# Kernel tuning notes

Measured on AMD Instinct MI355X. Metric: run time of the kernel, lower is better.

Reference implementation:

```python
import jax, jax.numpy as jnp
import numpy as np
from jax import lax

EPS = 1e-05


def rmsnorm_axis1(x, w, eps=EPS):
    # RMS over channel axis (axis=1), scale by per-channel weight
    ms = jnp.mean(x * x, axis=1, keepdims=True)
    return x * lax.rsqrt(ms + eps) * w[None, :, None]


def dwconv1d(x, w, b, dilation):
    # x: [B, C, L]; w: [C, 1, K] depthwise (feature_group_count=C)
    pad = (w.shape[-1] - 1) // 2 * dilation
    y = lax.conv_general_dilated(
        x, w, window_strides=(1,), padding=[(pad, pad)],
        rhs_dilation=(dilation,), dimension_numbers=('NCH', 'OIH', 'NCH'),
        feature_group_count=x.shape[1])
    return y + b[None, :, None]


def setup_inputs() -> dict:
    key = jax.random.key(0)
    ks = jax.random.split(key, 12)
    B, C, L, K = 16, 512, 2048, 3
    s = 1.0 / np.sqrt(C)
    return {
        'number_log': jax.random.normal(ks[0], (B,), jnp.float32),
        'x': jax.random.normal(ks[1], (B, C, L), jnp.float32),
        'pre_w': jnp.ones((C,), jnp.float32),
        'conv_w': jax.random.normal(ks[2], (C, 1, K), jnp.float32) * 0.3,
        'conv_b': jnp.zeros((C,), jnp.float32),
        'conv1_w': jax.random.normal(ks[3], (C, 1, K), jnp.float32) * 0.3,
        'conv1_b': jnp.zeros((C,), jnp.float32),
        'conv2_w': jax.random.normal(ks[4], (C, 1, K), jnp.float32) * 0.3,
        'conv2_b': jnp.zeros((C,), jnp.float32),
        'gate_w': jax.random.normal(ks[5], (C, C), jnp.float32) * s,
        'gate_b': jnp.zeros((C,), jnp.float32),
        'post_w': jnp.ones((C,), jnp.float32),
        'logits_w': jax.random.normal(ks[6], (1, C, 1), jnp.float32) * s,
    }


def reference(number_log, x, pre_w, conv_w, conv_b, conv1_w, conv1_b,
              conv2_w, conv2_b, gate_w, gate_b, post_w, logits_w):
    # pre_norm over channel axis
    x_norm = rmsnorm_axis1(x, pre_w)
    # three dilated depthwise conv branches, summed
    x_d = (dwconv1d(x_norm, conv_w, conv_b, 1)
           + dwconv1d(x_norm, conv1_w, conv1_b, 2)
           + dwconv1d(x_norm, conv2_w, conv2_b, 4))
    # gate: Linear over channel dim of transposed input, SiLU
    gate = jax.nn.silu(jnp.einsum('bcl,dc->bdl', x_norm, gate_w)
                       + gate_b[None, :, None])
    x_d = rmsnorm_axis1(x_d * gate, post_w)
    # logits: 1x1 conv C->1, no bias
    out = jnp.einsum('bcl,oc->bol', x + x_d, logits_w[:, :, 0])
    return out
```

## Files before the change

kernel.cpp:

```cpp
#include <hip/hip_runtime.h>
#include <hip/hip_bf16.h>

#define BB 16
#define CC 512
#define LL 2048

typedef float f32x4 __attribute__((ext_vector_type(4)));
typedef short s16x8 __attribute__((ext_vector_type(8)));

static __device__ __forceinline__ float bf2f(unsigned short u) {
    union { unsigned int i; float f; } v; v.i = ((unsigned int)u) << 16; return v.f;
}
static __device__ __forceinline__ unsigned short f2bf(float f) {
    union { float fv; unsigned int i; } v; v.fv = f;
    unsigned int x = v.i;
    return (unsigned short)((x + 0x7FFFu + ((x >> 16) & 1u)) >> 16);
}

__global__ void k0_cast(const float* __restrict__ gw, unsigned short* __restrict__ gwb) {
    int i = blockIdx.x * 256 + threadIdx.x;
    if (i < CC * CC) gwb[i] = f2bf(gw[i]);
}

#define K1_ST 520
__global__ __launch_bounds__(256) void k1_rms_t(
    const float* __restrict__ x, const float* __restrict__ pre_w,
    unsigned short* __restrict__ xnt, float* __restrict__ invr) {
    __shared__ unsigned short tile[32 * K1_ST];
    __shared__ float red[32 * 33];
    __shared__ float pwS[CC];
    __shared__ float ivS[32];
    const int tid = threadIdx.x;
    const int b  = blockIdx.x >> 6;
    const int lt = blockIdx.x & 63;
    const int l0 = lt * 32;
    const float* xb = x + (size_t)(b * CC) * LL + l0;

    for (int i = tid; i < CC; i += 256) pwS[i] = pre_w[i];

    const int lq = tid & 7;
    const int cr = tid >> 3;
    f32x4 ssq = {0.f, 0.f, 0.f, 0.f};
    #pragma unroll
    for (int p = 0; p < 16; ++p) {
        int c = p * 32 + cr;
        f32x4 v = *(const f32x4*)(xb + (size_t)c * LL + lq * 4);
        #pragma unroll
        for (int r = 0; r < 4; ++r) {
            ssq[r] += v[r] * v[r];
            tile[(lq * 4 + r) * K1_ST + c] = f2bf(v[r]);
        }
    }
    #pragma unroll
    for (int r = 0; r < 4; ++r) red[(lq * 4 + r) * 33 + cr] = ssq[r];
    __syncthreads();
    if (tid < 32) {
        float s = 0.f;
        #pragma unroll
        for (int g = 0; g < 32; ++g) s += red[tid * 33 + g];
        float iv = rsqrtf(s * (1.0f / CC) + 1e-5f);
        ivS[tid] = iv;
        invr[b * LL + l0 + tid] = iv;
    }
    __syncthreads();
    unsigned short* xo = xnt + ((size_t)b * LL + l0) * CC;
    #pragma unroll
    for (int p = 0; p < 8; ++p) {
        int g = p * 256 + tid;
        int l = g >> 6, c8 = (g & 63) * 8;
        s16x8 t = *(const s16x8*)&tile[l * K1_ST + c8];
        f32x4 w0 = *(const f32x4*)&pwS[c8];
        f32x4 w1 = *(const f32x4*)&pwS[c8 + 4];
        float iv = ivS[l];
        s16x8 o;
        #pragma unroll
        for (int r = 0; r < 4; ++r) {
            o[r]     = (short)f2bf(bf2f((unsigned short)t[r])     * iv * w0[r]);
            o[r + 4] = (short)f2bf(bf2f((unsigned short)t[r + 4]) * iv * w1[r]);
        }
        *(s16x8*)(xo + (size_t)l * CC + c8) = o;
    }
}

__global__ __launch_bounds__(512, 2) void k2_gemm(
    const unsigned short* __restrict__ gwb,
    const unsigned short* __restrict__ xnt,
    const float* __restrict__ gate_b,
    unsigned short* __restrict__ gate) {
    __shared__ unsigned short As[3][256 * 32];
    __shared__ unsigned short Bs[3][256 * 32];
    const int tid = threadIdx.x;
    const int w = tid >> 6, lane = tid & 63;
    const int lo = lane & 15, hi = lane >> 4;
    const int wm = w >> 2, wn = w & 3;
    const int nt = blockIdx.x, mt = blockIdx.y, b = blockIdx.z;
    const int m0 = mt * 256, n0 = nt * 256;
    const unsigned short* Ab = gwb;
    const unsigned short* Bb = xnt + (size_t)b * LL * CC;

    #define STG(kt_, buf_)                                                            \
        {                                                                             \
            _Pragma("unroll")                                                         \
            for (int s_ = 0; s_ < 2; ++s_) {                                          \
                int g_ = tid + s_ * 512;                                              \
                int row_ = g_ >> 2, gin_ = g_ & 3;                                    \
                int ks_ = (kt_) * 32 + ((gin_ ^ ((row_ >> 1) & 3)) * 8);              \
                __builtin_amdgcn_global_load_lds(                                     \
                    (const __attribute__((address_space(1))) void*)(Ab + (size_t)(m0 + row_) * CC + ks_), \
                    (__attribute__((address_space(3))) void*)(&As[buf_][g_ * 8]),     \
                    16, 0, 0);                                                        \
                __builtin_amdgcn_global_load_lds(                                     \
                    (const __attribute__((address_space(1))) void*)(Bb + (size_t)(n0 + row_) * CC + ks_), \
                    (__attribute__((address_space(3))) void*)(&Bs[buf_][g_ * 8]),     \
                    16, 0, 0);                                                        \
            }                                                                         \
        }

    f32x4 acc[8][4] = {};
    const int fsw = (lo >> 1) & 3;

    STG(0, 0);
    STG(1, 1);
    #pragma unroll
    for (int kt = 0; kt < 16; ++kt) {
        const int buf = kt % 3;
        if (kt < 14) {
            STG(kt + 2, (kt + 2) % 3);
            asm volatile("s_waitcnt vmcnt(8)" ::: "memory");
        } else if (kt == 14) {
            asm volatile("s_waitcnt vmcnt(4)" ::: "memory");
        } else {
            asm volatile("s_waitcnt vmcnt(0)" ::: "memory");
        }
        __builtin_amdgcn_s_barrier();
        s16x8 af[8], bfr[4];
        #pragma unroll
        for (int mi = 0; mi < 8; ++mi)
            af[mi] = *(const s16x8*)&As[buf][(wm * 128 + mi * 16 + lo) * 32 + ((hi ^ fsw) * 8)];
        #pragma unroll
        for (int ni = 0; ni < 4; ++ni)
            bfr[ni] = *(const s16x8*)&Bs[buf][(wn * 64 + ni * 16 + lo) * 32 + ((hi ^ fsw) * 8)];
        __builtin_amdgcn_s_setprio(1);
        #pragma unroll
        for (int mi = 0; mi < 8; ++mi)
            #pragma unroll
            for (int ni = 0; ni < 4; ++ni)
                acc[mi][ni] = __builtin_amdgcn_mfma_f32_16x16x32_bf16(
                    af[mi], bfr[ni], acc[mi][ni], 0, 0, 0);
        __builtin_amdgcn_s_setprio(0);
        asm volatile("" ::: "memory");
        __builtin_amdgcn_s_barrier();
    }
    #undef STG

    #pragma unroll
    for (int mi = 0; mi < 8; ++mi) {
        #pragma unroll
        for (int ni = 0; ni < 4; ++ni) {
            int n = n0 + wn * 64 + ni * 16 + lo;
            int d0 = m0 + wm * 128 + mi * 16 + hi * 4;
            #pragma unroll
            for (int r = 0; r < 4; ++r) {
                int d = d0 + r;
                float z = acc[mi][ni][r] + gate_b[d];
                float s = z / (1.0f + __expf(-z));
                gate[((size_t)(b * CC + d)) * LL + n] = f2bf(s);
            }
        }
    }
}

__global__ __launch_bounds__(256) void k3a(
    const float* __restrict__ x, const float* __restrict__ invr,
    const unsigned short* __restrict__ gate,
    const float* __restrict__ cw0, const float* __restrict__ cb0,
    const float* __restrict__ cw1, const float* __restrict__ cb1,
    const float* __restrict__ cw2, const float* __restrict__ cb2,
    const float* __restrict__ pre_w, const float* __restrict__ post_w,
    const float* __restrict__ lw, float* __restrict__ part) {
    __shared__ float tapS[64][8];
    __shared__ float biasS[64], preS[64], lwS[64], pwlwS[64];
    __shared__ float ivs[136];
    __shared__ float red[8][128][3];
    const int tid = threadIdx.x;
    const int lt = blockIdx.x;
    const int cc = blockIdx.y;
    const int b  = blockIdx.z;
    const int l0 = lt * 128;
    const int c0 = cc * 64;

    if (tid < 64) {
        int c = c0 + tid;
        float w10 = cw0[c*3], w11 = cw0[c*3+1], w12 = cw0[c*3+2];
        float w20 = cw1[c*3], w21 = cw1[c*3+1], w22 = cw1[c*3+2];
        float w40 = cw2[c*3], w41 = cw2[c*3+1], w42 = cw2[c*3+2];
        tapS[tid][0] = w40; tapS[tid][1] = w20; tapS[tid][2] = w10;
        tapS[tid][3] = w11 + w21 + w41;
        tapS[tid][4] = w12; tapS[tid][5] = w22; tapS[tid][6] = w42;
        biasS[tid] = cb0[c] + cb1[c] + cb2[c];
        preS[tid]  = pre_w[c];
        float lwc = lw[c];
        lwS[tid] = lwc;
        pwlwS[tid] = post_w[c] * lwc;
    }
    if (tid < 136) {
        int lg = l0 - 4 + tid;
        ivs[tid] = (lg >= 0 && lg < LL) ? invr[b * LL + lg] : 0.f;
    }
    __syncthreads();

    const int li = tid & 31, ci = tid >> 5;
    const int lq = l0 + li * 4;
    float iv[12];
    #pragma unroll
    for (int j = 0; j < 12; ++j) iv[j] = ivs[li * 4 + j];

    const int ia = (lq - 4 < 0) ? 0 : lq - 4;
    const int ic = (lq + 4 > LL - 4) ? LL - 4 : lq + 4;

    float ass[4] = {}, adp[4] = {}, adx[4] = {};
    const float* xbase = x + ((size_t)(b * CC + c0)) * LL;
    const unsigned short* gbase = gate + ((size_t)(b * CC + c0)) * LL;

    #pragma unroll
    for (int j = 0; j < 8; ++j) {
        const int cl = ci * 8 + j;
        const float* xr = xbase + (size_t)cl * LL;
        f32x4 xa = *(const f32x4*)(xr + ia);
        f32x4 xm = *(const f32x4*)(xr + lq);
        f32x4 xc = *(const f32x4*)(xr + ic);
        uint2 gu = *(const uint2*)(gbase + (size_t)cl * LL + lq);
        float g[4];
        g[0] = bf2f((unsigned short)(gu.x & 0xffff));
        g[1] = bf2f((unsigned short)(gu.x >> 16));
        g[2] = bf2f((unsigned short)(gu.y & 0xffff));
        g[3] = bf2f((unsigned short)(gu.y >> 16));
        float z[12];
        #pragma unroll
        for (int r = 0; r < 4; ++r) {
            z[r]     = xa[r] * iv[r];
            z[r + 4] = xm[r] * iv[r + 4];
            z[r + 8] = xc[r] * iv[r + 8];
        }
        const float t0 = tapS[cl][0], t1 = tapS[cl][1], t2 = tapS[cl][2],
                    t3 = tapS[cl][3], t4 = tapS[cl][4], t5 = tapS[cl][5],
                    t6 = tapS[cl][6];
        const float pre = preS[cl], bias = biasS[cl], pwlw = pwlwS[cl], lwc = lwS[cl];
        #pragma unroll
        for (int k = 0; k < 4; ++k) {
            float s = t0 * z[k] + t1 * z[k + 2] + t2 * z[k + 3] + t3 * z[k + 4]
                    + t4 * z[k + 5] + t5 * z[k + 6] + t6 * z[k + 8];
            float p = (pre * s + bias) * g[k];
            ass[k] += p * p;
            adp[k] += p * pwlw;
            adx[k] += xm[k] * lwc;
        }
    }
    #pragma unroll
    for (int k = 0; k < 4; ++k) {
        red[ci][li * 4 + k][0] = ass[k];
        red[ci][li * 4 + k][1] = adp[k];
        red[ci][li * 4 + k][2] = adx[k];
    }
    __syncthreads();
    if (tid < 128) {
        float s0 = 0.f, s1 = 0.f, s2 = 0.f;
        #pragma unroll
        for (int g2 = 0; g2 < 8; ++g2) {
            s0 += red[g2][tid][0];
            s1 += red[g2][tid][1];
            s2 += red[g2][tid][2];
        }
        float* pp = part + (((size_t)(b * 8 + cc)) * LL + l0 + tid) * 3;
        pp[0] = s0; pp[1] = s1; pp[2] = s2;
    }
}

__global__ __launch_bounds__(256) void k3b(
    const float* __restrict__ part, float* __restrict__ out) {
    int gl = blockIdx.x * 256 + threadIdx.x;
    int b = gl >> 11, l = gl & 2047;
    float s0 = 0.f, s1 = 0.f, s2 = 0.f;
    #pragma unroll
    for (int cc2 = 0; cc2 < 8; ++cc2) {
        const float* pp = part + (((size_t)(b * 8 + cc2)) * LL + l) * 3;
        s0 += pp[0]; s1 += pp[1]; s2 += pp[2];
    }
    out[gl] = s2 + rsqrtf(s0 * (1.0f / CC) + 1e-5f) * s1;
}

extern "C" void kernel_launch(void* const* d_in, const int* in_sizes, int n_in,
                              void* d_out, int out_size, void* d_ws, size_t ws_size,
                              hipStream_t stream) {
    const float* x      = (const float*)d_in[1];
    const float* pre_w  = (const float*)d_in[2];
    const float* cw0    = (const float*)d_in[3];
    const float* cb0    = (const float*)d_in[4];
    const float* cw1    = (const float*)d_in[5];
    const float* cb1    = (const float*)d_in[6];
    const float* cw2    = (const float*)d_in[7];
    const float* cb2    = (const float*)d_in[8];
    const float* gw     = (const float*)d_in[9];
    const float* gb     = (const float*)d_in[10];
    const float* post_w = (const float*)d_in[11];
    const float* lw     = (const float*)d_in[12];
    float* out = (float*)d_out;

    char* ws = (char*)d_ws;
    unsigned short* gwb  = (unsigned short*)(ws);
    unsigned short* xnt  = (unsigned short*)(ws + 524288);
    float*          invr = (float*)(ws + 524288 + 33554432);
    unsigned short* gate = (unsigned short*)(ws + 524288 + 33554432 + 131072);
    float*          part = (float*)(ws + 524288);

    hipLaunchKernelGGL(k0_cast,  dim3((CC * CC + 255) / 256), dim3(256), 0, stream, gw, gwb);
    hipLaunchKernelGGL(k1_rms_t, dim3(BB * (LL / 32)),        dim3(256), 0, stream, x, pre_w, xnt, invr);
    hipLaunchKernelGGL(k2_gemm,  dim3(LL / 256, CC / 256, BB), dim3(512), 0, stream, gwb, xnt, gb, gate);
    hipLaunchKernelGGL(k3a,      dim3(LL / 128, CC / 64, BB), dim3(256), 0, stream,
                       x, invr, gate, cw0, cb0, cw1, cb1, cw2, cb2, pre_w, post_w, lw, part);
    hipLaunchKernelGGL(k3b,      dim3(BB * LL / 256),         dim3(256), 0, stream, part, out);
}
```

Baseline: 78.64 us.

## Restructure gate GEMM into 8-phase pipeline with K=64 tiles and interleaved staging

Replaces the triple-buffered K=32 main loop of the gate GEMM with double-buffered K=64 tiles split into half-tiles. Each K-step runs as four phases, and each phase loads a slice of A fragments, issues one global-to-LDS stage, and performs a burst of MFMAs. This spreads memory issue across compute phases, widens the XOR LDS swizzle to 8 groups, and halves the number of barrier-delimited K iterations per tile. The cost is more barriers per K-step and tighter hand-tuned vmcnt accounting, which risks hazards if the counts are wrong.

```diff
diff --git a/kernel.cpp b/kernel.cpp
--- a/kernel.cpp
+++ b/kernel.cpp
@@ -87,8 +87,8 @@
     const unsigned short* __restrict__ xnt,
     const float* __restrict__ gate_b,
     unsigned short* __restrict__ gate) {
-    __shared__ unsigned short As[3][256 * 32];
-    __shared__ unsigned short Bs[3][256 * 32];
+    __shared__ unsigned short Ash[2][2][128 * 64];
+    __shared__ unsigned short Bsh[2][2][128 * 64];
     const int tid = threadIdx.x;
     const int w = tid >> 6, lane = tid & 63;
     const int lo = lane & 15, hi = lane >> 4;
@@ -98,60 +98,94 @@
     const unsigned short* Ab = gwb;
     const unsigned short* Bb = xnt + (size_t)b * LL * CC;
 
-    #define STG(kt_, buf_)                                                            \
+    const int srow = tid >> 3;
+    const int skg  = tid & 7;
+
+    #define STGA(d_, h_, kt_)                                                         \
+        { _Pragma("unroll")                                                           \
+          for (int s_ = 0; s_ < 2; ++s_) {                                            \
+              int row_ = srow + s_ * 64;                                              \
+              __builtin_amdgcn_global_load_lds(                                       \
+                  (const __attribute__((address_space(1))) void*)(Ab + (size_t)(m0 + (h_) * 128 + row_) * CC + (kt_) * 64 + ((skg ^ (row_ & 7)) * 8)), \
+                  (__attribute__((address_space(3))) void*)(&Ash[d_][h_][(row_ * 8 + skg) * 8]), \
+                  16, 0, 0);                                                          \
+          } }
+    #define STGB(d_, h_, kt_)                                                         \
+        { _Pragma("unroll")                                                           \
+          for (int s_ = 0; s_ < 2; ++s_) {                                            \
+              int row_ = srow + s_ * 64;                                              \
+              __builtin_amdgcn_global_load_lds(                                       \
+                  (const __attribute__((address_space(1))) void*)(Bb + (size_t)(n0 + (h_) * 128 + row_) * CC + (kt_) * 64 + ((skg ^ (row_ & 7)) * 8)), \
+                  (__attribute__((address_space(3))) void*)(&Bsh[d_][h_][(row_ * 8 + skg) * 8]), \
+                  16, 0, 0);                                                          \
+          } }
+
+    f32x4 acc[8][4] = {};
+
+    STGA(0, 0, 0); STGA(0, 1, 0);
+    STGB(0, 0, 0); STGB(0, 1, 0);
+    STGB(1, 0, 1); STGB(1, 1, 1);
+    asm volatile("s_waitcnt vmcnt(0)" ::: "memory");
+    __builtin_amdgcn_s_barrier();
+
+    #define PHASE(d_, q_, STAGE_STMT, VM_STMT)                                        \
         {                                                                             \
+            s16x8 af_[2][2];                                                          \
             _Pragma("unroll")                                                         \
-            for (int s_ = 0; s_ < 2; ++s_) {                                          \
-                int g_ = tid + s_ * 512;                                              \
-                int row_ = g_ >> 2, gin_ = g_ & 3;                                    \
-                int ks_ = (kt_) * 32 + ((gin_ ^ ((row_ >> 1) & 3)) * 8);              \
-                __builtin_amdgcn_global_load_lds(                                     \
-                    (const __attribute__((address_space(1))) void*)(Ab + (size_t)(m0 + row_) * CC + ks_), \
-                    (__attribute__((address_space(3))) void*)(&As[buf_][g_ * 8]),     \
-                    16, 0, 0);                                                        \
-                __builtin_amdgcn_global_load_lds(                                     \
-                    (const __attribute__((address_space(1))) void*)(Bb + (size_t)(n0 + row_) * CC + ks_), \
-                    (__attribute__((address_space(3))) void*)(&Bs[buf_][g_ * 8]),     \
-                    16, 0, 0);                                                        \
+            for (int j_ = 0; j_ < 2; ++j_) {                                          \
+                int lr_ = ((q_) * 2 + j_) * 16 + lo;                                  \
+                _Pragma("unroll")                                                     \
+                for (int kk_ = 0; kk_ < 2; ++kk_)                                     \
+                    af_[j_][kk_] = *(const s16x8*)&Ash[d_][wm][lr_ * 64 + (((kk_ * 4 + hi) ^ (lr_ & 7)) * 8)]; \
             }                                                                         \
-        }
-
-    f32x4 acc[8][4] = {};
-    const int fsw = (lo >> 1) & 3;
-
-    STG(0, 0);
-    STG(1, 1);
-    #pragma unroll
-    for (int kt = 0; kt < 16; ++kt) {
-        const int buf = kt % 3;
-        if (kt < 14) {
-            STG(kt + 2, (kt + 2) % 3);
-            asm volatile("s_waitcnt vmcnt(8)" ::: "memory");
-        } else if (kt == 14) {
-            asm volatile("s_waitcnt vmcnt(4)" ::: "memory");
-        } else {
-            asm volatile("s_waitcnt vmcnt(0)" ::: "memory");
-        }
-        __builtin_amdgcn_s_barrier();
-        s16x8 af[8], bfr[4];
-        #pragma unroll
-        for (int mi = 0; mi < 8; ++mi)
-            af[mi] = *(const s16x8*)&As[buf][(wm * 128 + mi * 16 + lo) * 32 + ((hi ^ fsw) * 8)];
-        #pragma unroll
-        for (int ni = 0; ni < 4; ++ni)
-            bfr[ni] = *(const s16x8*)&Bs[buf][(wn * 64 + ni * 16 + lo) * 32 + ((hi ^ fsw) * 8)];
-        __builtin_amdgcn_s_setprio(1);
-        #pragma unroll
-        for (int mi = 0; mi < 8; ++mi)
-            #pragma unroll
-            for (int ni = 0; ni < 4; ++ni)
-                acc[mi][ni] = __builtin_amdgcn_mfma_f32_16x16x32_bf16(
-                    af[mi], bfr[ni], acc[mi][ni], 0, 0, 0);
-        __builtin_amdgcn_s_setprio(0);
-        asm volatile("" ::: "memory");
-        __builtin_amdgcn_s_barrier();
-    }
-    #undef STG
+            if ((q_) == 0) {                                                          \
+                _Pragma("unroll")                                                     \
+                for (int ni_ = 0; ni_ < 4; ++ni_) {                                   \
+                    int gr_ = wn * 64 + ni_ * 16 + lo;                                \
+                    int lr_ = gr_ & 127;                                              \
+                    _Pragma("unroll")                                                 \
+                    for (int kk_ = 0; kk_ < 2; ++kk_)                                 \
+                        bfr[ni_][kk_] = *(const s16x8*)&Bsh[d_][gr_ >> 7][lr_ * 64 + (((kk_ * 4 + hi) ^ (lr_ & 7)) * 8)]; \
+                }                                                                     \
+            }                                                                         \
+            STAGE_STMT;                                                               \
+            __builtin_amdgcn_s_barrier();                                             \
+            asm volatile("s_waitcnt lgkmcnt(0)" ::: "memory");                        \
+            __builtin_amdgcn_sched_barrier(0);                                        \
+            __builtin_amdgcn_s_setprio(1);                                            \
+            _Pragma("unroll")                                                         \
+            for (int j_ = 0; j_ < 2; ++j_)                                            \
+                _Pragma("unroll")                                                     \
+                for (int ni_ = 0; ni_ < 4; ++ni_)                                     \
+                    _Pragma("unroll")                                                 \
+                    for (int kk_ = 0; kk_ < 2; ++kk_)                                 \
+                        acc[(q_) * 2 + j_][ni_] = __builtin_amdgcn_mfma_f32_16x16x32_bf16( \
+                            af_[j_][kk_], bfr[ni_][kk_], acc[(q_) * 2 + j_][ni_], 0, 0, 0); \
+            __builtin_amdgcn_s_setprio(0);                                            \
+            VM_STMT;                                                                  \
+            __builtin_amdgcn_s_barrier();                                             \
+        }
+
+    #define VM4  asm volatile("s_waitcnt vmcnt(4)" ::: "memory")
+    #define VM0  asm volatile("s_waitcnt vmcnt(0)" ::: "memory")
+
+    #pragma unroll
+    for (int I = 0; I < 4; ++I) {
+        s16x8 bfr[4][2];
+        PHASE(0, 0, STGA(1, 0, 2 * I + 1), );
+        PHASE(0, 1, STGA(1, 1, 2 * I + 1), );
+        PHASE(0, 2, if (I < 3) STGB(0, 0, 2 * I + 2), );
+        PHASE(0, 3, if (I < 3) STGB(0, 1, 2 * I + 2), if (I < 3) { VM4; } else { VM0; });
+        PHASE(1, 0, if (I < 3) STGA(0, 0, 2 * I + 2), );
+        PHASE(1, 1, if (I < 3) STGA(0, 1, 2 * I + 2), );
+        PHASE(1, 2, if (I < 3) STGB(1, 0, 2 * I + 3), );
+        PHASE(1, 3, if (I < 3) STGB(1, 1, 2 * I + 3), if (I < 3) { VM4; });
+    }
+    #undef PHASE
+    #undef STGA
+    #undef STGB
+    #undef VM4
+    #undef VM0
 
     #pragma unroll
     for (int mi = 0; mi < 8; ++mi) {
```

Measured after the change: 80.50 us. 1.02x slower.
